# Performance work log

Hardware: AMD Instinct MI355X
Metric: run time of the kernel (lower is better)

## Reference

```python
import jax, jax.numpy as jnp
from jax import lax
import numpy as np

DIM = 384
NUM_HEADS = 8
HEAD_DIM = DIM // NUM_HEADS


def setup_inputs() -> dict:
    key = jax.random.key(0)
    k_x, k_qw, k_qb, k_lw, k_lb = jax.random.split(key, 5)
    B, H, W = 2, 64, 64
    N = H * W
    x = jax.random.normal(k_x, (B, N, DIM), dtype=jnp.float32)
    # nn.Linear(dim, 3*dim): weight (3C, C), bias (3C,)
    qkv_w = jax.random.normal(k_qw, (3 * DIM, DIM), dtype=jnp.float32) * (1.0 / np.sqrt(DIM))
    qkv_b = jax.random.normal(k_qb, (3 * DIM,), dtype=jnp.float32) * 0.02
    # nn.Conv2d(dim, dim, 3, padding=1, groups=dim): weight (C, 1, 3, 3), bias (C,)
    lepe_w = jax.random.normal(k_lw, (DIM, 1, 3, 3), dtype=jnp.float32) * (1.0 / 3.0)
    lepe_b = jax.random.normal(k_lb, (DIM,), dtype=jnp.float32) * 0.02
    return {"x": x, "qkv_w": qkv_w, "qkv_b": qkv_b, "lepe_w": lepe_w, "lepe_b": lepe_b, "H": H, "W": W}


def reference(x, qkv_w, qkv_b, lepe_w, lepe_b, H, W):
    B, N, C = x.shape
    hd = C // NUM_HEADS
    scale = hd ** -0.5
    # qkv projection: (B, N, 3C) -> (B, N, 3, heads, head_dim)
    qkv = (jnp.einsum('bnc,oc->bno', x, qkv_w) + qkv_b).reshape(B, N, 3, NUM_HEADS, hd)
    q, k, v = qkv[:, :, 0], qkv[:, :, 1], qkv[:, :, 2]  # each (B, N, heads, hd)
    attn = jnp.einsum('bnhd,bmhd->bhnm', q * scale, k)   # (B, heads, N, N)
    attn = jax.nn.softmax(attn, axis=-1)
    out = jnp.einsum('bhnm,bmhd->bnhd', attn, v).reshape(B, N, C)
    # LePE: depthwise 3x3 conv on v in NCHW layout
    v_img = v.reshape(B, H, W, C).transpose(0, 3, 1, 2)  # (B, C, H, W)
    lepe = lax.conv_general_dilated(
        v_img, lepe_w, window_strides=(1, 1), padding='SAME',
        feature_group_count=C,
        dimension_numbers=('NCHW', 'OIHW', 'NCHW'))
    lepe = lepe + lepe_b[None, :, None, None]
    return out + lepe.transpose(0, 2, 3, 1).reshape(B, N, C)
```

## Files before the change

kernel.cpp:

```cpp
#include <hip/hip_runtime.h>
#include <stdint.h>

#define DIM   384
#define NH    8
#define HD    48
#define NTOK  4096
#define KDIM  384
#define SCALEL2E 0.20823509610f

typedef float  f32x4   __attribute__((ext_vector_type(4)));
typedef float  f32x16  __attribute__((ext_vector_type(16)));
typedef __bf16 bf16x8  __attribute__((ext_vector_type(8)));

#if __has_builtin(__builtin_amdgcn_exp2f)
#define EXP2F(x) __builtin_amdgcn_exp2f(x)
#else
#define EXP2F(x) exp2f(x)
#endif

__device__ __forceinline__ unsigned short f2bf(float f) {
  union { float f; unsigned int u; } c; c.f = f;
  unsigned int r = (c.u + 0x7FFFu + ((c.u >> 16) & 1u)) >> 16;
  return (unsigned short)r;
}
__device__ __forceinline__ float bf2f(unsigned short h) {
  union { unsigned int u; float f; } c; c.u = ((unsigned int)h) << 16;
  return c.f;
}


__global__ void prep_kernel(const float* __restrict__ x, const float* __restrict__ w,
                            unsigned short* __restrict__ x_bf,
                            unsigned short* __restrict__ w_bf) {
  int tid = blockIdx.x * blockDim.x + threadIdx.x;
  int stride = gridDim.x * blockDim.x;
  for (int i = tid; i < 786432; i += stride) {
    float4 v = ((const float4*)x)[i];
    ushort4 o;
    o.x = f2bf(v.x); o.y = f2bf(v.y); o.z = f2bf(v.z); o.w = f2bf(v.w);
    ((ushort4*)x_bf)[i] = o;
  }
  for (int i = tid; i < 110592; i += stride) {
    float4 v = ((const float4*)w)[i];
    ushort4 o;
    o.x = f2bf(v.x); o.y = f2bf(v.y); o.z = f2bf(v.z); o.w = f2bf(v.w);
    ((ushort4*)w_bf)[i] = o;
  }
}

__global__ __launch_bounds__(256) void qkv_gemm(
    const unsigned short* __restrict__ A,
    const unsigned short* __restrict__ Bw,
    const float* __restrict__ bias,
    unsigned short* __restrict__ qc,
    unsigned short* __restrict__ kc,
    unsigned short* __restrict__ v_t) {
  __shared__ unsigned short ldsA[128 * 32];
  __shared__ unsigned short ldsB[64 * 32];
  __shared__ unsigned short ebuf[64 * 72];
  const int tid = threadIdx.x;
  const int wv = tid >> 6, ln = tid & 63;
  const int lrow = ln & 15, lq = ln >> 4;
  const int m0 = blockIdx.x * 128;
  const int n0 = blockIdx.y * 64;
  const int wm = (wv >> 1) * 64, wn = (wv & 1) * 32;

  f32x4 acc[4][2];
#pragma unroll
  for (int mi = 0; mi < 4; ++mi)
#pragma unroll
    for (int ni = 0; ni < 2; ++ni)
#pragma unroll
      for (int r = 0; r < 4; ++r) acc[mi][ni][r] = 0.f;

  for (int k0 = 0; k0 < KDIM; k0 += 32) {
    __syncthreads();
#pragma unroll
    for (int j = 0; j < 2; ++j) {
      int r16 = wv * 2 + j;
      const unsigned short* ga = A + (size_t)(m0 + r16 * 16 + (ln >> 2)) * KDIM
                                   + k0 + (ln & 3) * 8;
      __builtin_amdgcn_global_load_lds(
          (const __attribute__((address_space(1))) void*)ga,
          (__attribute__((address_space(3))) void*)&ldsA[r16 * 512], 16, 0, 0);
    }
    const unsigned short* gb = Bw + (size_t)(n0 + wv * 16 + (ln >> 2)) * KDIM
                                  + k0 + (ln & 3) * 8;
    __builtin_amdgcn_global_load_lds(
        (const __attribute__((address_space(1))) void*)gb,
        (__attribute__((address_space(3))) void*)&ldsB[wv * 512], 16, 0, 0);
    __syncthreads();
    bf16x8 af[4], bfv[2];
#pragma unroll
    for (int mi = 0; mi < 4; ++mi)
      af[mi] = *(const bf16x8*)&ldsA[(wm + mi * 16 + lrow) * 32 + lq * 8];
#pragma unroll
    for (int ni = 0; ni < 2; ++ni)
      bfv[ni] = *(const bf16x8*)&ldsB[(wn + ni * 16 + lrow) * 32 + lq * 8];
#pragma unroll
    for (int mi = 0; mi < 4; ++mi)
#pragma unroll
      for (int ni = 0; ni < 2; ++ni)
        acc[mi][ni] = __builtin_amdgcn_mfma_f32_16x16x32_bf16(
            af[mi], bfv[ni], acc[mi][ni], 0, 0, 0);
  }

  const int region = (n0 >= 768) ? 2 : (n0 >= 384 ? 1 : 0);
  const float scl = (region == 0) ? SCALEL2E : 1.0f;
  const float bias0 = bias[n0 + wn + lrow];
  const float bias1 = bias[n0 + wn + 16 + lrow];

#pragma unroll
  for (int half = 0; half < 2; ++half) {
    __syncthreads();
    if ((wv >> 1) == half) {
#pragma unroll
      for (int mi = 0; mi < 4; ++mi)
#pragma unroll
        for (int ni = 0; ni < 2; ++ni)
#pragma unroll
          for (int r = 0; r < 4; ++r) {
            int row = mi * 16 + lq * 4 + r;
            int col = wn + ni * 16 + lrow;
            float val = (acc[mi][ni][r] + (ni ? bias1 : bias0)) * scl;
            ebuf[row * 72 + col] = f2bf(val);
          }
    }
    __syncthreads();
    if (region < 2) {
      unsigned short* dst = (region == 0) ? qc : kc;
      const int obase = n0 - region * 384;
#pragma unroll
      for (int i = 0; i < 2; ++i) {
        int id = tid + i * 256;
        int row = id >> 3, cc = id & 7;
        uint4 val = *(const uint4*)&ebuf[row * 72 + cc * 8];
        int nrow = m0 + half * 64 + row;
        int b = nrow >> 12, nn = nrow & 4095;
        int o = obase + cc * 8;
        int h = o / 48, d = o - h * 48;
        *(uint4*)&dst[((size_t)(b * 8 + h) * NTOK + nn) * HD + d] = val;
      }
    } else {
#pragma unroll
      for (int i = 0; i < 2; ++i) {
        int id = tid + i * 256;
        int col = id & 63, rc = id >> 6;
        int r0 = rc * 8;
        union { unsigned short s[8]; uint4 u; } pk;
#pragma unroll
        for (int j = 0; j < 8; ++j)
          pk.s[j] = ebuf[(r0 + j) * 72 + col];
        int nrow = m0 + half * 64 + r0;
        int b = nrow >> 12;
        int o = n0 - 768 + col;
        *(uint4*)&v_t[((size_t)(b * DIM + o)) * NTOK + (nrow & 4095)] = pk.u;
      }
    }
  }
}

__global__ __launch_bounds__(256) void lepe_kernel(
    const unsigned short* __restrict__ v_t,
    const float* __restrict__ lw, const float* __restrict__ lb,
    float* __restrict__ out) {
  __shared__ __align__(16) unsigned short pl[16 * 648];
  const int cg = blockIdx.x;
  const int sy = blockIdx.y;
  const int b  = blockIdx.z;
  const int t = threadIdx.x;
  const int y0 = sy * 8;
#pragma unroll
  for (int i = 0; i < 5; ++i) {
    int id = t + i * 256;
    int c = id / 80, rem = id - c * 80;
    int row = rem >> 3, cx = rem & 7;
    int y = y0 - 1 + row;
    uint4 val = make_uint4(0u, 0u, 0u, 0u);
    if (y >= 0 && y < 64)
      val = *(const uint4*)(v_t + ((size_t)(b * DIM + cg * 16 + c)) * NTOK + y * 64 + cx * 8);
    *(uint4*)&pl[c * 648 + row * 64 + cx * 8] = val;
  }
  __syncthreads();
  const int c = t & 15, pg = t >> 4;
  const int cglob = cg * 16 + c;
  float w[9];
#pragma unroll
  for (int j = 0; j < 9; ++j) w[j] = lw[cglob * 9 + j];
  const float bias = lb[cglob];
  const unsigned short* base = &pl[c * 648];
  for (int i = 0; i < 32; ++i) {
    int p = pg * 32 + i;
    int lr = p >> 6, x = p & 63;
    float acc = bias;
#pragma unroll
    for (int ky = 0; ky < 3; ++ky)
#pragma unroll
      for (int kx = 0; kx < 3; ++kx) {
        int xx = x + kx - 1;
        if (xx >= 0 && xx < 64)
          acc += w[ky * 3 + kx] * bf2f(base[(lr + ky) * 64 + xx]);
      }
    out[((size_t)(b * NTOK + sy * 512 + p)) * DIM + cglob] = acc;
  }
}

__global__ __launch_bounds__(256, 2) void attn_kernel(
    const unsigned short* __restrict__ qc,
    const unsigned short* __restrict__ kcg,
    const unsigned short* __restrict__ v_t,
    float* __restrict__ out) {
  __shared__ __align__(16) char smem[33792];
  unsigned short* Kl = (unsigned short*)smem;
  unsigned short* Vl = (unsigned short*)(smem + 16384);
  float* Lsum = (float*)(smem + 32768);
  float* Ol   = (float*)smem;

  const int tid = threadIdx.x;
  const int wv = tid >> 6, ln = tid & 63;
  const int kh = wv >> 1;
  const int wq = wv & 1;
  const int l31 = ln & 31, hh = ln >> 5;
  const int th = tid & 127;
  const int qb = blockIdx.x;
  const int bh = blockIdx.y;
  const int b = bh >> 3, hd = bh & 7;

  unsigned short* Kh = Kl + kh * 4096;
  unsigned short* Vh = Vl + kh * 4096;

  int kro[4], kgo[4], vro[3], vgo[3];
#pragma unroll
  for (int i = 0; i < 4; ++i) {
    int idx = th + i * 128;
    int r = idx >> 3, cc = idx & 7;
    kro[i] = r * 64 + ((cc ^ (r & 7)) * 8);
    kgo[i] = r * 48 + cc * 8;
  }
#pragma unroll
  for (int i = 0; i < 3; ++i) {
    int idx = th + i * 128;
    int vd = idx >> 3, vc = idx & 7;
    vro[i] = vd * 64 + ((vc ^ (vd & 7)) * 8);
    vgo[i] = vd * 4096 + vc * 8;
  }

  if (th < 8) {
    uint4 one4 = make_uint4(0x3F803F80u, 0x3F803F80u, 0x3F803F80u, 0x3F803F80u);
    *(uint4*)&Vh[3072 + th * 8] = one4;
  }

  bf16x8 Qf[2][3];
#pragma unroll
  for (int set = 0; set < 2; ++set) {
    const int qrow = qb * 128 + set * 64 + wq * 32 + l31;
    const unsigned short* qp = qc + ((size_t)bh * NTOK + qrow) * HD + hh * 8;
#pragma unroll
    for (int hs = 0; hs < 3; ++hs)
      Qf[set][hs] = *(const bf16x8*)(qp + hs * 16);
  }

  f32x16 Oacc[2][2];
#pragma unroll
  for (int set = 0; set < 2; ++set)
#pragma unroll
    for (int dc = 0; dc < 2; ++dc)
#pragma unroll
      for (int r = 0; r < 16; ++r) Oacc[set][dc][r] = 0.f;

  const unsigned short* kbase = kcg + (size_t)bh * NTOK * HD;
  const unsigned short* vbase = v_t + ((size_t)b * DIM + hd * HD) * NTOK;

  for (int it = 0; it < 32; ++it) {
    const int kt = kh * 32 + it;
    __syncthreads();
    const unsigned short* kg = kbase + (size_t)kt * 64 * HD;
    const unsigned short* vg = vbase + kt * 64;
#pragma unroll
    for (int i = 0; i < 4; ++i)
      *(uint4*)&Kh[kro[i]] = *(const uint4*)(kg + kgo[i]);
#pragma unroll
    for (int i = 0; i < 3; ++i)
      *(uint4*)&Vh[vro[i]] = *(const uint4*)(vg + vgo[i]);
    __syncthreads();

    unsigned int P32[2][16];
#pragma unroll
    for (int C = 0; C < 2; ++C) {
      f32x16 sA, sB;
#pragma unroll
      for (int r = 0; r < 16; ++r) { sA[r] = 0.f; sB[r] = 0.f; }
      const int krow = C * 32 + l31;
      const unsigned short* kr = &Kh[krow * 64];
      const int rx = krow & 7;
#pragma unroll
      for (int hs = 0; hs < 3; ++hs) {
        bf16x8 kf = *(const bf16x8*)&kr[((hs * 2 + hh) ^ rx) * 8];
        sA = __builtin_amdgcn_mfma_f32_32x32x16_bf16(kf, Qf[0][hs], sA, 0, 0, 0);
        sB = __builtin_amdgcn_mfma_f32_32x32x16_bf16(kf, Qf[1][hs], sB, 0, 0, 0);
      }
#pragma unroll
      for (int t8 = 0; t8 < 8; ++t8) {
        float a0 = EXP2F(sA[2 * t8]);
        float a1 = EXP2F(sA[2 * t8 + 1]);
        P32[0][C * 8 + t8] = __builtin_amdgcn_perm(
            __float_as_uint(a1), __float_as_uint(a0), 0x07060302u);
        float b0 = EXP2F(sB[2 * t8]);
        float b1 = EXP2F(sB[2 * t8 + 1]);
        P32[1][C * 8 + t8] = __builtin_amdgcn_perm(
            __float_as_uint(b1), __float_as_uint(b0), 0x07060302u);
      }
    }

#pragma unroll
    for (int s4 = 0; s4 < 4; ++s4) {
      bf16x8 vf[2];
#pragma unroll
      for (int dc = 0; dc < 2; ++dc) {
        int vrow = dc * 32 + l31;
        vf[dc] = *(const bf16x8*)&Vh[vrow * 64 + (((s4 * 2 + hh) ^ (vrow & 7)) * 8)];
      }
      const int o = (s4 >> 1) * 8 + (s4 & 1) * 4;
#pragma unroll
      for (int set = 0; set < 2; ++set) {
        unsigned int send1 = hh ? P32[set][o + 0] : P32[set][o + 2];
        unsigned int send2 = hh ? P32[set][o + 1] : P32[set][o + 3];
        unsigned int recv1 = (unsigned int)__shfl_xor((int)send1, 32, 64);
        unsigned int recv2 = (unsigned int)__shfl_xor((int)send2, 32, 64);
        union { unsigned int u[4]; bf16x8 v; } pa;
        pa.u[0] = hh ? recv1 : P32[set][o + 0];
        pa.u[1] = hh ? recv2 : P32[set][o + 1];
        pa.u[2] = hh ? P32[set][o + 2] : recv1;
        pa.u[3] = hh ? P32[set][o + 3] : recv2;
#pragma unroll
        for (int dc = 0; dc < 2; ++dc)
          Oacc[set][dc] = __builtin_amdgcn_mfma_f32_32x32x16_bf16(
              pa.v, vf[dc], Oacc[set][dc], 0, 0, 0);
      }
    }
  }

  __syncthreads();
  if (l31 == 16) {
#pragma unroll
    for (int set = 0; set < 2; ++set)
#pragma unroll
      for (int r = 0; r < 16; ++r) {
        int qrb = set * 64 + wq * 32 + (r & 3) + 8 * (r >> 2) + 4 * hh;
        Lsum[kh * 128 + qrb] = Oacc[set][1][r];
      }
  }
  if (kh == 1) {
#pragma unroll
    for (int set = 0; set < 2; ++set)
#pragma unroll
      for (int r = 0; r < 16; ++r) {
        int qrb = set * 64 + wq * 32 + (r & 3) + 8 * (r >> 2) + 4 * hh;
        Ol[qrb * 48 + l31] = Oacc[set][0][r];
        if (l31 < 16) Ol[qrb * 48 + 32 + l31] = Oacc[set][1][r];
      }
  }
  __syncthreads();
  if (kh == 0) {
#pragma unroll
    for (int set = 0; set < 2; ++set)
#pragma unroll
      for (int r = 0; r < 16; ++r) {
        int qrb = set * 64 + wq * 32 + (r & 3) + 8 * (r >> 2) + 4 * hh;
        float linv = 1.0f / (Lsum[qrb] + Lsum[128 + qrb]);
        float* op = out + ((size_t)(b * NTOK + qb * 128 + qrb)) * DIM + hd * HD;
        op[l31] += (Oacc[set][0][r] + Ol[qrb * 48 + l31]) * linv;
        if (l31 < 16)
          op[32 + l31] += (Oacc[set][1][r] + Ol[qrb * 48 + 32 + l31]) * linv;
      }
  }
}

extern "C" void kernel_launch(void* const* d_in, const int* in_sizes, int n_in,
                              void* d_out, int out_size, void* d_ws, size_t ws_size,
                              hipStream_t stream) {
  const float* x      = (const float*)d_in[0];
  const float* qkv_w  = (const float*)d_in[1];
  const float* qkv_b  = (const float*)d_in[2];
  const float* lepe_w = (const float*)d_in[3];
  const float* lepe_b = (const float*)d_in[4];

  char* ws = (char*)d_ws;
  unsigned short* x_bf = (unsigned short*)(ws);
  unsigned short* w_bf = (unsigned short*)(ws + 6291456);
  unsigned short* qcp  = (unsigned short*)(ws + 7176192);
  unsigned short* kcp  = (unsigned short*)(ws + 13467648);
  unsigned short* v_t  = (unsigned short*)(ws + 19759104);
  float* out = (float*)d_out;

  prep_kernel<<<1024, 256, 0, stream>>>(x, qkv_w, x_bf, w_bf);
  qkv_gemm<<<dim3(64, 18), 256, 0, stream>>>(x_bf, w_bf, qkv_b, qcp, kcp, v_t);
  lepe_kernel<<<dim3(24, 8, 2), 256, 0, stream>>>(v_t, lepe_w, lepe_b, out);
  attn_kernel<<<dim3(32, 16), 256, 0, stream>>>(qcp, kcp, v_t, out);
}
```

Before: 207.7 us.

## Prefetch K/V tiles into registers and remove P cross-lane shuffles

The global loads for the next K/V tile now go into registers while the current tile is being computed, so load latency overlaps the MFMA work. LDS layout switches from XOR swizzle to padded rows (stride 72 for K, 68 for V), and V is read as two 8-byte pieces matching the P register layout. This removes the __shfl_xor exchange of probabilities, and each 32-key chunk's P is consumed by the PV MFMAs right after it is computed. The cost is more LDS, extra registers for the prefetch buffers, and a redundant wrap-around load on the last iteration.

```diff
diff --git a/kernel.cpp b/kernel.cpp
--- a/kernel.cpp
+++ b/kernel.cpp
@@ -210,10 +210,10 @@
     const unsigned short* __restrict__ kcg,
     const unsigned short* __restrict__ v_t,
     float* __restrict__ out) {
-  __shared__ __align__(16) char smem[33792];
+  __shared__ __align__(16) char smem[36864];
   unsigned short* Kl = (unsigned short*)smem;
-  unsigned short* Vl = (unsigned short*)(smem + 16384);
-  float* Lsum = (float*)(smem + 32768);
+  unsigned short* Vl = (unsigned short*)(smem + 18432);
+  float* Lsum = (float*)(smem + 35840);
   float* Ol   = (float*)smem;
 
   const int tid = threadIdx.x;
@@ -226,28 +226,28 @@
   const int bh = blockIdx.y;
   const int b = bh >> 3, hd = bh & 7;
 
-  unsigned short* Kh = Kl + kh * 4096;
-  unsigned short* Vh = Vl + kh * 4096;
-
-  int kro[4], kgo[4], vro[3], vgo[3];
+  unsigned short* Kh = Kl + kh * 4608;
+  unsigned short* Vh = Vl + kh * 4352;
+
+  int kwo[4], kgo[4], vwo[3], vgo[3];
 #pragma unroll
   for (int i = 0; i < 4; ++i) {
     int idx = th + i * 128;
     int r = idx >> 3, cc = idx & 7;
-    kro[i] = r * 64 + ((cc ^ (r & 7)) * 8);
+    kwo[i] = r * 72 + cc * 8;
     kgo[i] = r * 48 + cc * 8;
   }
 #pragma unroll
   for (int i = 0; i < 3; ++i) {
     int idx = th + i * 128;
     int vd = idx >> 3, vc = idx & 7;
-    vro[i] = vd * 64 + ((vc ^ (vd & 7)) * 8);
+    vwo[i] = vd * 68 + vc * 8;
     vgo[i] = vd * 4096 + vc * 8;
   }
 
   if (th < 8) {
     uint4 one4 = make_uint4(0x3F803F80u, 0x3F803F80u, 0x3F803F80u, 0x3F803F80u);
-    *(uint4*)&Vh[3072 + th * 8] = one4;
+    *(uint4*)&Vh[48 * 68 + th * 8] = one4;
   }
 
   bf16x8 Qf[2][3];
@@ -271,71 +271,78 @@
   const unsigned short* kbase = kcg + (size_t)bh * NTOK * HD;
   const unsigned short* vbase = v_t + ((size_t)b * DIM + hd * HD) * NTOK;
 
+  uint4 kreg[4], vreg[3];
+  {
+    const unsigned short* kg = kbase + (size_t)(kh * 32) * 64 * HD;
+    const unsigned short* vg = vbase + (kh * 32) * 64;
+#pragma unroll
+    for (int i = 0; i < 4; ++i) kreg[i] = *(const uint4*)(kg + kgo[i]);
+#pragma unroll
+    for (int i = 0; i < 3; ++i) vreg[i] = *(const uint4*)(vg + vgo[i]);
+  }
+
   for (int it = 0; it < 32; ++it) {
-    const int kt = kh * 32 + it;
-    __syncthreads();
-    const unsigned short* kg = kbase + (size_t)kt * 64 * HD;
-    const unsigned short* vg = vbase + kt * 64;
-#pragma unroll
-    for (int i = 0; i < 4; ++i)
-      *(uint4*)&Kh[kro[i]] = *(const uint4*)(kg + kgo[i]);
-#pragma unroll
-    for (int i = 0; i < 3; ++i)
-      *(uint4*)&Vh[vro[i]] = *(const uint4*)(vg + vgo[i]);
-    __syncthreads();
-
-    unsigned int P32[2][16];
+    __syncthreads();
+#pragma unroll
+    for (int i = 0; i < 4; ++i) *(uint4*)&Kh[kwo[i]] = kreg[i];
+#pragma unroll
+    for (int i = 0; i < 3; ++i) *(uint4*)&Vh[vwo[i]] = vreg[i];
+    {
+      int ktn = kh * 32 + ((it + 1) & 31);
+      const unsigned short* kg = kbase + (size_t)ktn * 64 * HD;
+      const unsigned short* vg = vbase + ktn * 64;
+#pragma unroll
+      for (int i = 0; i < 4; ++i) kreg[i] = *(const uint4*)(kg + kgo[i]);
+#pragma unroll
+      for (int i = 0; i < 3; ++i) vreg[i] = *(const uint4*)(vg + vgo[i]);
+    }
+    __syncthreads();
+
 #pragma unroll
     for (int C = 0; C < 2; ++C) {
       f32x16 sA, sB;
 #pragma unroll
       for (int r = 0; r < 16; ++r) { sA[r] = 0.f; sB[r] = 0.f; }
-      const int krow = C * 32 + l31;
-      const unsigned short* kr = &Kh[krow * 64];
-      const int rx = krow & 7;
+      const unsigned short* kr = &Kh[(C * 32 + l31) * 72 + hh * 8];
 #pragma unroll
       for (int hs = 0; hs < 3; ++hs) {
-        bf16x8 kf = *(const bf16x8*)&kr[((hs * 2 + hh) ^ rx) * 8];
+        bf16x8 kf = *(const bf16x8*)(kr + hs * 16);
         sA = __builtin_amdgcn_mfma_f32_32x32x16_bf16(kf, Qf[0][hs], sA, 0, 0, 0);
         sB = __builtin_amdgcn_mfma_f32_32x32x16_bf16(kf, Qf[1][hs], sB, 0, 0, 0);
       }
+      unsigned int PA[8], PB[8];
 #pragma unroll
       for (int t8 = 0; t8 < 8; ++t8) {
         float a0 = EXP2F(sA[2 * t8]);
         float a1 = EXP2F(sA[2 * t8 + 1]);
-        P32[0][C * 8 + t8] = __builtin_amdgcn_perm(
-            __float_as_uint(a1), __float_as_uint(a0), 0x07060302u);
+        PA[t8] = __builtin_amdgcn_perm(__float_as_uint(a1), __float_as_uint(a0),
+                                       0x07060302u);
         float b0 = EXP2F(sB[2 * t8]);
         float b1 = EXP2F(sB[2 * t8 + 1]);
-        P32[1][C * 8 + t8] = __builtin_amdgcn_perm(
-            __float_as_uint(b1), __float_as_uint(b0), 0x07060302u);
-      }
-    }
-
-#pragma unroll
-    for (int s4 = 0; s4 < 4; ++s4) {
-      bf16x8 vf[2];
-#pragma unroll
-      for (int dc = 0; dc < 2; ++dc) {
-        int vrow = dc * 32 + l31;
-        vf[dc] = *(const bf16x8*)&Vh[vrow * 64 + (((s4 * 2 + hh) ^ (vrow & 7)) * 8)];
-      }
-      const int o = (s4 >> 1) * 8 + (s4 & 1) * 4;
-#pragma unroll
-      for (int set = 0; set < 2; ++set) {
-        unsigned int send1 = hh ? P32[set][o + 0] : P32[set][o + 2];
-        unsigned int send2 = hh ? P32[set][o + 1] : P32[set][o + 3];
-        unsigned int recv1 = (unsigned int)__shfl_xor((int)send1, 32, 64);
-        unsigned int recv2 = (unsigned int)__shfl_xor((int)send2, 32, 64);
-        union { unsigned int u[4]; bf16x8 v; } pa;
-        pa.u[0] = hh ? recv1 : P32[set][o + 0];
-        pa.u[1] = hh ? recv2 : P32[set][o + 1];
-        pa.u[2] = hh ? P32[set][o + 2] : recv1;
-        pa.u[3] = hh ? P32[set][o + 3] : recv2;
-#pragma unroll
-        for (int dc = 0; dc < 2; ++dc)
-          Oacc[set][dc] = __builtin_amdgcn_mfma_f32_32x32x16_bf16(
-              pa.v, vf[dc], Oacc[set][dc], 0, 0, 0);
+        PB[t8] = __builtin_amdgcn_perm(__float_as_uint(b1), __float_as_uint(b0),
+                                       0x07060302u);
+      }
+#pragma unroll
+      for (int u = 0; u < 2; ++u) {
+        union { unsigned int w[4]; bf16x8 v; } pa0, pa1;
+#pragma unroll
+        for (int w4 = 0; w4 < 4; ++w4) {
+          pa0.w[w4] = PA[4 * u + w4];
+          pa1.w[w4] = PB[4 * u + w4];
+        }
+        const int goff = (C * 8 + 4 * u + hh) * 4;
+#pragma unroll
+        for (int dc = 0; dc < 2; ++dc) {
+          const int vrow = dc * 32 + l31;
+          const unsigned short* vrp = &Vh[vrow * 68 + goff];
+          union { uint2 x[2]; bf16x8 v; } vf;
+          vf.x[0] = *(const uint2*)(vrp);
+          vf.x[1] = *(const uint2*)(vrp + 8);
+          Oacc[0][dc] = __builtin_amdgcn_mfma_f32_32x32x16_bf16(
+              pa0.v, vf.v, Oacc[0][dc], 0, 0, 0);
+          Oacc[1][dc] = __builtin_amdgcn_mfma_f32_32x32x16_bf16(
+              pa1.v, vf.v, Oacc[1][dc], 0, 0, 0);
+        }
       }
     }
   }
```

Measured after the change: 254.3 us. 22.4% more time.
